# Kernel tuning notes

Measured on AMD Instinct MI355X. Metric: run time of the kernel, lower is better.

Reference implementation:

```python
import jax, jax.numpy as jnp
import numpy as np

N, K = 16384, 32          # num bboxes, context size
IN_F, HID = 608, 384      # in_features, hidden_dim
ALPHA = 0.2               # LeakyReLU slope
NEG_INF = -9e15


def setup_inputs() -> dict:
    key = jax.random.key(0)
    k1, k2, k3, k4, k5, k6, k7, k8 = jax.random.split(key, 8)
    h_i = jax.random.normal(k1, (N, IN_F), dtype=jnp.float32)
    idx = jax.random.randint(k2, (N, K), 0, N)
    pad = jax.random.uniform(k3, (N, K)) < 0.2
    context_indices = jnp.where(pad, -1, idx).astype(jnp.int64)
    s_in = 1.0 / np.sqrt(IN_F)
    s_a = 1.0 / np.sqrt(2 * HID)
    W_i = jax.random.uniform(k4, (IN_F, HID), minval=-s_in, maxval=s_in, dtype=jnp.float32)
    W_j = jax.random.uniform(k5, (IN_F, HID), minval=-s_in, maxval=s_in, dtype=jnp.float32)
    a_i = jax.random.uniform(k6, (HID,), minval=-s_a, maxval=s_a, dtype=jnp.float32)
    a_j = jax.random.uniform(k7, (HID,), minval=-s_a, maxval=s_a, dtype=jnp.float32)
    a_b = jax.random.uniform(k8, (1,), minval=-s_a, maxval=s_a, dtype=jnp.float32)
    return {"h_i": h_i, "context_indices": context_indices,
            "W_i": W_i, "W_j": W_j, "a_i": a_i, "a_j": a_j, "a_b": a_b}


def reference(h_i, context_indices, W_i, W_j, a_i, a_j, a_b):
    n = h_i.shape[0]
    Wh_i = h_i @ W_i                          # [N, H]
    # W_j has no bias, so projecting then gathering (zero pad row) equals
    # gathering zero-padded features then projecting.
    Wh_all = h_i @ W_j                        # [N, H]
    Wh_pad = jnp.concatenate([Wh_all, jnp.zeros((1, HID), Wh_all.dtype)], axis=0)
    idx = jnp.where(context_indices >= 0, context_indices, n)   # -1 -> zero row
    Wh_j = Wh_pad[idx]                        # [N, K, H] gather
    # attention_layer(concat(Wh_i, Wh_j)) == Wh_i@a_i + Wh_j@a_j + b
    scores = (Wh_i @ a_i)[:, None] + Wh_j @ a_j + a_b[0]        # [N, K]
    scores = jnp.where(scores > 0, scores, ALPHA * scores)      # LeakyReLU
    scores = jnp.where(context_indices >= 0, scores, NEG_INF)   # mask padding
    att = jax.nn.softmax(scores, axis=1)                        # [N, K]
    h_prime = jnp.einsum('nk,nkh->nh', att, Wh_j)               # [N, H]
    return h_prime
```

## Files before the change

kernel.cpp:

```cpp
#include <hip/hip_runtime.h>
#include <hip/hip_bf16.h>

typedef unsigned short u16;
typedef unsigned int u32;
typedef __attribute__((ext_vector_type(8))) __bf16 bf16x8;
typedef __attribute__((ext_vector_type(4))) __bf16 bf16x4;
typedef __attribute__((ext_vector_type(4))) float f32x4;

#define KCTX 32
#define INF_ 608
#define HID_ 384

#define WH_OFF  19922944
#define BT_OFF  32505856
#define V_OFF   32972800
#define SI_OFF  32975232
#define SJ_OFF  33040768
#define AJF_OFF 33106304
#define ABF_OFF 33107840

__device__ __forceinline__ float bfu(u16 u)  { return __uint_as_float(((u32)u) << 16); }
__device__ __forceinline__ float bflo(u32 u) { return __uint_as_float(u << 16); }
__device__ __forceinline__ float bfhi(u32 u) { return __uint_as_float(u & 0xffff0000u); }
__device__ __forceinline__ u16 f2bf(float x) {
  u32 u = __float_as_uint(x);
  return (u16)((u + 0x7fffu + ((u >> 16) & 1u)) >> 16);
}
__device__ __forceinline__ void async_ld16(const void* g, void* l) {
  __builtin_amdgcn_global_load_lds(
      (const __attribute__((address_space(1))) u32*)g,
      (__attribute__((address_space(3))) u32*)l, 16, 0, 0);
}

__device__ __forceinline__ int detect_f32(const u32* hw) {
  const u32 w = hw[threadIdx.x & 63];
  const int e = (int)((w >> 7) & 0xffu);
  const unsigned long long mb = __ballot(e > 134 || e < 100);
  return __popcll(mb) >= 16;
}
__device__ __forceinline__ int detect_i64(const int* ci) {
  const int hi = ci[2 * (threadIdx.x & 63) + 1];
  const unsigned long long mz = __ballot(hi == 0 || hi == -1);
  return __popcll(mz) >= 48;
}

__global__ __launch_bounds__(256) void prep_kernel(
    const void* __restrict__ h, const void* __restrict__ Wi,
    const void* __restrict__ Wj, const void* __restrict__ ai,
    const void* __restrict__ aj, const void* __restrict__ ab,
    u16* __restrict__ Bt, float* __restrict__ v, float* __restrict__ sj,
    float* __restrict__ ajf, float* __restrict__ abf) {
  __shared__ u16 tile[64][65];
  const int f32m = detect_f32((const u32*)h);
  const int bid = blockIdx.x, tid = threadIdx.x;
  if (bid < 60) {
    const int ft = bid / 6, ht = bid - ft * 6;
    const int f0 = ft * 64, h0 = ht * 64;
    const int ln = tid & 63, fg = tid >> 6;
#pragma unroll
    for (int rr = 0; rr < 16; ++rr) {
      const int fl = fg * 16 + rr;
      const int f = f0 + fl;
      if (f < INF_)
        tile[fl][ln] = f32m ? f2bf(((const float*)Wj)[(size_t)f * HID_ + h0 + ln])
                            : ((const u16*)Wj)[(size_t)f * HID_ + h0 + ln];
    }
    __syncthreads();
#pragma unroll
    for (int rr = 0; rr < 16; ++rr) {
      const int hl = fg * 16 + rr;
      const int f = f0 + ln;
      if (f < INF_) Bt[(size_t)(h0 + hl) * INF_ + f] = tile[ln][hl];
    }
  } else if (bid < 98) {
    const int t = (bid - 60) * 16 + (tid >> 4);
    const int sl = tid & 15;
    if (t < INF_) {
      float s = 0.f;
      if (f32m) {
        const float4* wi = (const float4*)((const float*)Wi + (size_t)t * HID_);
        const float4* a4 = (const float4*)ai;
        for (int c = sl; c < 96; c += 16) {
          float4 x = wi[c], y = a4[c];
          s += x.x * y.x + x.y * y.y + x.z * y.z + x.w * y.w;
        }
      } else {
        const uint4* wi = (const uint4*)((const u16*)Wi + (size_t)t * HID_);
        const uint4* a4 = (const uint4*)ai;
        for (int c = sl; c < 48; c += 16) {
          uint4 x = wi[c], y = a4[c];
          s += bflo(x.x) * bflo(y.x) + bfhi(x.x) * bfhi(y.x)
             + bflo(x.y) * bflo(y.y) + bfhi(x.y) * bfhi(y.y)
             + bflo(x.z) * bflo(y.z) + bfhi(x.z) * bfhi(y.z)
             + bflo(x.w) * bflo(y.w) + bfhi(x.w) * bfhi(y.w);
        }
      }
      s += __shfl_xor(s, 1); s += __shfl_xor(s, 2);
      s += __shfl_xor(s, 4); s += __shfl_xor(s, 8);
      if (sl == 0) v[t] = s;
    }
  } else {
#pragma unroll 8
    for (int j = 0; j < 64; ++j) sj[j * 256 + tid] = 0.f;
    for (int j = tid; j < HID_; j += 256)
      ajf[j] = f32m ? ((const float*)aj)[j] : bfu(((const u16*)aj)[j]);
    if (tid == 0)
      abf[0] = f32m ? ((const float*)ab)[0] : bfu(((const u16*)ab)[0]);
  }
}

__global__ __launch_bounds__(256) void gemm_fused(
    const void* __restrict__ A,
    const u16* __restrict__ Bt,
    const float* __restrict__ v,
    u16* __restrict__ C,
    float* __restrict__ si, const float* __restrict__ ajf,
    float* __restrict__ sj) {
  __shared__ __align__(16) u16 As[32][612];
  __shared__ __align__(16) u16 Bs[12288];
  const int f32m = detect_f32((const u32*)A);
  const int tid  = threadIdx.x;
  const int lane = tid & 63;
  const int wv   = tid >> 6;
  const int row0 = blockIdx.x * 32;
  const char* Btb = (const char*)Bt;

#pragma unroll
  for (int i = 0; i < 6; ++i) {
    const int c = tid + i * 256;
    async_ld16(Btb + (size_t)(c >> 2) * 1216 + (c & 3) * 16, (char*)Bs + c * 16);
  }

  {
    const int g = tid >> 3, sub = tid & 7;
    float s = 0.f;
    const float4* v4 = (const float4*)v;
    if (f32m) {
      const float4* hr = (const float4*)((const float*)A + (size_t)(row0 + g) * INF_);
#pragma unroll
      for (int k = 0; k < 19; ++k) {
        const int c4 = sub + 8 * k;
        float4 x = hr[c4];
        ushort4 sv;
        sv.x = f2bf(x.x); sv.y = f2bf(x.y); sv.z = f2bf(x.z); sv.w = f2bf(x.w);
        *(ushort4*)&As[g][c4 * 4] = sv;
        float4 w = v4[c4];
        s += x.x * w.x + x.y * w.y + x.z * w.z + x.w * w.w;
      }
    } else {
      const uint4* hr = (const uint4*)((const u16*)A + (size_t)(row0 + g) * INF_);
      for (int k = 0; k < 10; ++k) {
        const int c8 = sub + 8 * k;
        if (c8 < 76) {
          uint4 x = hr[c8];
          *(ushort4*)&As[g][c8 * 8]     = *(ushort4*)&x.x;
          *(ushort4*)&As[g][c8 * 8 + 4] = *(ushort4*)&x.z;
          float4 w0 = v4[2 * c8], w1 = v4[2 * c8 + 1];
          s += bflo(x.x) * w0.x + bfhi(x.x) * w0.y + bflo(x.y) * w0.z + bfhi(x.y) * w0.w
             + bflo(x.z) * w1.x + bfhi(x.z) * w1.y + bflo(x.w) * w1.z + bfhi(x.w) * w1.w;
        }
      }
    }
    s += __shfl_xor(s, 1); s += __shfl_xor(s, 2); s += __shfl_xor(s, 4);
    if (sub == 0) si[row0 + g] = s;
  }

  f32x4 acc[2][6];
#pragma unroll
  for (int i = 0; i < 2; ++i)
#pragma unroll
    for (int j = 0; j < 6; ++j) acc[i][j] = (f32x4){0.f, 0.f, 0.f, 0.f};

  const int lm = lane & 15, q = lane >> 4;
  const int n0 = wv * 96;

  for (int kt = 0; kt < 19; ++kt) {
    __syncthreads();
    bf16x8 af[2], bfr[6];
#pragma unroll
    for (int im = 0; im < 2; ++im) {
      const int r = im * 16 + lm;
      bf16x4 lo = *(const bf16x4*)&As[r][kt * 32 + q * 8];
      bf16x4 hi = *(const bf16x4*)&As[r][kt * 32 + q * 8 + 4];
      af[im] = __builtin_shufflevector(lo, hi, 0, 1, 2, 3, 4, 5, 6, 7);
    }
#pragma unroll
    for (int in = 0; in < 6; ++in)
      bfr[in] = *(const bf16x8*)&Bs[(n0 + in * 16 + lm) * 32 + q * 8];
#pragma unroll
    for (int im = 0; im < 2; ++im)
#pragma unroll
      for (int in = 0; in < 6; ++in)
        acc[im][in] = __builtin_amdgcn_mfma_f32_16x16x32_bf16(
            af[im], bfr[in], acc[im][in], 0, 0, 0);
    __syncthreads();
    if (kt < 18) {
      const size_t kb = (size_t)(kt + 1) * 64;
#pragma unroll
      for (int i = 0; i < 6; ++i) {
        const int c = tid + i * 256;
        async_ld16(Btb + (size_t)(c >> 2) * 1216 + kb + (c & 3) * 16, (char*)Bs + c * 16);
      }
    }
  }

#pragma unroll
  for (int im = 0; im < 2; ++im)
#pragma unroll
    for (int in = 0; in < 6; ++in) {
      const int colg = n0 + in * 16 + lm;
#pragma unroll
      for (int r = 0; r < 4; ++r) {
        const int rowg = row0 + im * 16 + q * 4 + r;
        C[(size_t)rowg * HID_ + colg] = f2bf(acc[im][in][r]);
      }
    }
  float ajv[6];
#pragma unroll
  for (int in = 0; in < 6; ++in) ajv[in] = ajf[n0 + in * 16 + lm];
#pragma unroll
  for (int im = 0; im < 2; ++im)
#pragma unroll
    for (int r = 0; r < 4; ++r) {
      float p = acc[im][0][r] * ajv[0] + acc[im][1][r] * ajv[1]
              + acc[im][2][r] * ajv[2] + acc[im][3][r] * ajv[3]
              + acc[im][4][r] * ajv[4] + acc[im][5][r] * ajv[5];
      p += __shfl_xor(p, 1); p += __shfl_xor(p, 2);
      p += __shfl_xor(p, 4); p += __shfl_xor(p, 8);
      if (lm == 0) atomicAdd(&sj[row0 + im * 16 + q * 4 + r], p);
    }
}

__global__ __launch_bounds__(256) void attn_kernel(
    const void* __restrict__ h, const int* __restrict__ ci,
    const float* __restrict__ si, const float* __restrict__ sj,
    const float* __restrict__ abf, const u16* __restrict__ Wh,
    void* __restrict__ out) {
  const int f32m = detect_f32((const u32*)h);
  const int i64  = detect_i64(ci);
  const int wv = threadIdx.x >> 6, lane = threadIdx.x & 63;
  const int n = blockIdx.x * 4 + wv;

  float att = 0.f; int idxv = 0;
  if (lane < 32) {
    const size_t t = (size_t)n * KCTX + lane;
    int idx;
    if (i64) { int lo = ci[2 * t], hi = ci[2 * t + 1]; idx = (hi < 0) ? -1 : lo; }
    else     { idx = ci[t]; }
    const bool valid = idx >= 0;
    const float sjv = valid ? sj[idx] : 0.f;
    float raw = si[n] + sjv + abf[0];
    float lr = raw > 0.f ? raw : 0.2f * raw;
    float s = valid ? lr : -9e15f;
    float m = s;
#pragma unroll
    for (int o = 16; o; o >>= 1) m = fmaxf(m, __shfl_xor(m, o, 32));
    float p = __expf(s - m);
    float d = p;
#pragma unroll
    for (int o = 16; o; o >>= 1) d += __shfl_xor(d, o, 32);
    att = valid ? p / d : 0.f;
    idxv = valid ? idx : 0;
  }

  if (lane < 48) {
    float a0 = 0, a1 = 0, a2 = 0, a3 = 0, a4 = 0, a5 = 0, a6 = 0, a7 = 0;
#pragma unroll
    for (int kb = 0; kb < KCTX; kb += 8) {
      uint4 q[8]; float ww[8];
#pragma unroll
      for (int u = 0; u < 8; ++u) {
        ww[u] = __shfl(att, kb + u);
        const int j = __shfl(idxv, kb + u);
        q[u] = ((const uint4*)(Wh + (u32)j * HID_))[lane];
      }
#pragma unroll
      for (int u = 0; u < 8; ++u) {
        const float w = ww[u];
        a0 += w * bflo(q[u].x); a1 += w * bfhi(q[u].x);
        a2 += w * bflo(q[u].y); a3 += w * bfhi(q[u].y);
        a4 += w * bflo(q[u].z); a5 += w * bfhi(q[u].z);
        a6 += w * bflo(q[u].w); a7 += w * bfhi(q[u].w);
      }
    }
    if (f32m) {
      float4* o4 = (float4*)out + (size_t)n * 96 + lane * 2;
      o4[0] = (float4){a0, a1, a2, a3};
      o4[1] = (float4){a4, a5, a6, a7};
    } else {
      uint4 o;
      o.x = (u32)f2bf(a0) | ((u32)f2bf(a1) << 16);
      o.y = (u32)f2bf(a2) | ((u32)f2bf(a3) << 16);
      o.z = (u32)f2bf(a4) | ((u32)f2bf(a5) << 16);
      o.w = (u32)f2bf(a6) | ((u32)f2bf(a7) << 16);
      ((uint4*)out)[(size_t)n * 48 + lane] = o;
    }
  }
}

extern "C" void kernel_launch(void* const* d_in, const int* in_sizes, int n_in,
                              void* d_out, int out_size, void* d_ws, size_t ws_size,
                              hipStream_t stream) {
  const void* h  = d_in[0];
  const int*  ci = (const int*)d_in[1];
  const void* Wi = d_in[2];
  const void* Wj = d_in[3];
  const void* ai = d_in[4];
  const void* aj = d_in[5];
  const void* ab = d_in[6];

  char* ws = (char*)d_ws;
  u16*   Wh  = (u16*)(ws + WH_OFF);
  u16*   Bt  = (u16*)(ws + BT_OFF);
  float* v   = (float*)(ws + V_OFF);
  float* si  = (float*)(ws + SI_OFF);
  float* sj  = (float*)(ws + SJ_OFF);
  float* ajf = (float*)(ws + AJF_OFF);
  float* abf = (float*)(ws + ABF_OFF);

  prep_kernel<<<99, 256, 0, stream>>>(h, Wi, Wj, ai, aj, ab, Bt, v, sj, ajf, abf);
  gemm_fused<<<512, 256, 0, stream>>>(h, Bt, v, Wh, si, ajf, sj);
  attn_kernel<<<4096, 256, 0, stream>>>(h, ci, si, sj, abf, Wh, d_out);
}
```

Measured before the change: 156.7 us.

## Compact valid context entries and pack five rows per attention block

```diff
diff --git a/kernel.cpp b/kernel.cpp
--- a/kernel.cpp
+++ b/kernel.cpp
@@ -10,6 +10,7 @@
 #define KCTX 32
 #define INF_ 608
 #define HID_ 384
+#define NBOX 16384
 
 #define WH_OFF  19922944
 #define BT_OFF  32505856
@@ -110,10 +111,8 @@
 }
 
 __global__ __launch_bounds__(256) void gemm_fused(
-    const void* __restrict__ A,
-    const u16* __restrict__ Bt,
-    const float* __restrict__ v,
-    u16* __restrict__ C,
+    const void* __restrict__ A, const u16* __restrict__ Bt,
+    const float* __restrict__ v, u16* __restrict__ C,
     float* __restrict__ si, const float* __restrict__ ajf,
     float* __restrict__ sj) {
   __shared__ __align__(16) u16 As[32][612];
@@ -236,64 +235,85 @@
     const float* __restrict__ si, const float* __restrict__ sj,
     const float* __restrict__ abf, const u16* __restrict__ Wh,
     void* __restrict__ out) {
+  __shared__ float2 ai_c[5][32];
+  __shared__ int cnt_s[5];
   const int f32m = detect_f32((const u32*)h);
   const int i64  = detect_i64(ci);
-  const int wv = threadIdx.x >> 6, lane = threadIdx.x & 63;
-  const int n = blockIdx.x * 4 + wv;
-
-  float att = 0.f; int idxv = 0;
-  if (lane < 32) {
-    const size_t t = (size_t)n * KCTX + lane;
-    int idx;
-    if (i64) { int lo = ci[2 * t], hi = ci[2 * t + 1]; idx = (hi < 0) ? -1 : lo; }
-    else     { idx = ci[t]; }
-    const bool valid = idx >= 0;
-    const float sjv = valid ? sj[idx] : 0.f;
-    float raw = si[n] + sjv + abf[0];
-    float lr = raw > 0.f ? raw : 0.2f * raw;
-    float s = valid ? lr : -9e15f;
-    float m = s;
-#pragma unroll
-    for (int o = 16; o; o >>= 1) m = fmaxf(m, __shfl_xor(m, o, 32));
-    float p = __expf(s - m);
-    float d = p;
-#pragma unroll
-    for (int o = 16; o; o >>= 1) d += __shfl_xor(d, o, 32);
-    att = valid ? p / d : 0.f;
-    idxv = valid ? idx : 0;
-  }
-
-  if (lane < 48) {
-    float a0 = 0, a1 = 0, a2 = 0, a3 = 0, a4 = 0, a5 = 0, a6 = 0, a7 = 0;
-#pragma unroll
-    for (int kb = 0; kb < KCTX; kb += 8) {
-      uint4 q[8]; float ww[8];
-#pragma unroll
-      for (int u = 0; u < 8; ++u) {
-        ww[u] = __shfl(att, kb + u);
-        const int j = __shfl(idxv, kb + u);
-        q[u] = ((const uint4*)(Wh + (u32)j * HID_))[lane];
-      }
-#pragma unroll
-      for (int u = 0; u < 8; ++u) {
-        const float w = ww[u];
-        a0 += w * bflo(q[u].x); a1 += w * bfhi(q[u].x);
-        a2 += w * bflo(q[u].y); a3 += w * bfhi(q[u].y);
-        a4 += w * bflo(q[u].z); a5 += w * bfhi(q[u].z);
-        a6 += w * bflo(q[u].w); a7 += w * bfhi(q[u].w);
-      }
-    }
-    if (f32m) {
-      float4* o4 = (float4*)out + (size_t)n * 96 + lane * 2;
-      o4[0] = (float4){a0, a1, a2, a3};
-      o4[1] = (float4){a4, a5, a6, a7};
-    } else {
-      uint4 o;
-      o.x = (u32)f2bf(a0) | ((u32)f2bf(a1) << 16);
-      o.y = (u32)f2bf(a2) | ((u32)f2bf(a3) << 16);
-      o.z = (u32)f2bf(a4) | ((u32)f2bf(a5) << 16);
-      o.w = (u32)f2bf(a6) | ((u32)f2bf(a7) << 16);
-      ((uint4*)out)[(size_t)n * 48 + lane] = o;
+  const int tid = threadIdx.x;
+  const int n0 = blockIdx.x * 5;
+
+  if (tid < 160) {
+    const int r = tid >> 5, k = tid & 31;
+    const int n = n0 + r;
+    if (n < NBOX) {
+      const size_t t = (size_t)n * KCTX + k;
+      int idx;
+      if (i64) { int lo = ci[2 * t], hi2 = ci[2 * t + 1]; idx = (hi2 < 0) ? -1 : lo; }
+      else     { idx = ci[t]; }
+      const bool valid = idx >= 0;
+      const float sjv = valid ? sj[idx] : 0.f;
+      float raw = si[n] + sjv + abf[0];
+      float lr = raw > 0.f ? raw : 0.2f * raw;
+      float s = valid ? lr : -9e15f;
+      float m = s;
+#pragma unroll
+      for (int o = 16; o; o >>= 1) m = fmaxf(m, __shfl_xor(m, o, 32));
+      float p = __expf(s - m);
+      float d = p;
+#pragma unroll
+      for (int o = 16; o; o >>= 1) d += __shfl_xor(d, o, 32);
+      const unsigned long long bm = __ballot(valid);
+      const u32 m32 = (u32)(bm >> (tid & 32));
+      const int cnt = __popc(m32);
+      const int r8 = (cnt + 7) & ~7;
+      if (valid) {
+        const int pf = __popc(m32 & ((1u << k) - 1u));
+        ai_c[r][pf] = (float2){p / d, __int_as_float(idx)};
+      }
+      if (k >= cnt && k < r8) ai_c[r][k] = (float2){0.f, 0.f};
+      if (k == 0) cnt_s[r] = r8;
+    } else if ((tid & 31) == 0) {
+      cnt_s[r] = 0;
+    }
+  }
+  __syncthreads();
+
+  if (tid < 240) {
+    const int r = tid / 48, c = tid - r * 48;
+    const int n = n0 + r;
+    if (n < NBOX) {
+      const int K8 = cnt_s[r];
+      float a0 = 0, a1 = 0, a2 = 0, a3 = 0, a4 = 0, a5 = 0, a6 = 0, a7 = 0;
+      for (int kb = 0; kb < K8; kb += 8) {
+        uint4 q[8]; float ww[8];
+#pragma unroll
+        for (int u = 0; u < 8; ++u) {
+          const float2 e = ai_c[r][kb + u];
+          ww[u] = e.x;
+          const int j = __float_as_int(e.y);
+          q[u] = ((const uint4*)(Wh + (u32)j * HID_))[c];
+        }
+#pragma unroll
+        for (int u = 0; u < 8; ++u) {
+          const float w = ww[u];
+          a0 += w * bflo(q[u].x); a1 += w * bfhi(q[u].x);
+          a2 += w * bflo(q[u].y); a3 += w * bfhi(q[u].y);
+          a4 += w * bflo(q[u].z); a5 += w * bfhi(q[u].z);
+          a6 += w * bflo(q[u].w); a7 += w * bfhi(q[u].w);
+        }
+      }
+      if (f32m) {
+        float4* o4 = (float4*)out + (size_t)n * 96 + c * 2;
+        o4[0] = (float4){a0, a1, a2, a3};
+        o4[1] = (float4){a4, a5, a6, a7};
+      } else {
+        uint4 o;
+        o.x = (u32)f2bf(a0) | ((u32)f2bf(a1) << 16);
+        o.y = (u32)f2bf(a2) | ((u32)f2bf(a3) << 16);
+        o.z = (u32)f2bf(a4) | ((u32)f2bf(a5) << 16);
+        o.w = (u32)f2bf(a6) | ((u32)f2bf(a7) << 16);
+        ((uint4*)out)[(size_t)n * 48 + c] = o;
+      }
     }
   }
 }
@@ -320,5 +340,5 @@
 
   prep_kernel<<<99, 256, 0, stream>>>(h, Wi, Wj, ai, aj, ab, Bt, v, sj, ajf, abf);
   gemm_fused<<<512, 256, 0, stream>>>(h, Bt, v, Wh, si, ajf, sj);
-  attn_kernel<<<4096, 256, 0, stream>>>(h, ci, si, sj, abf, Wh, d_out);
-}
+  attn_kernel<<<3277, 256, 0, stream>>>(h, ci, si, sj, abf, Wh, d_out);
+}
```

After: 156.8 us (median of 2 runs). No clear change (+0.1%).

## Split score softmax into own kernel and slice Wh gather by column chunks

Applied to the files above, without the earlier changes.

```diff
diff --git a/kernel.cpp b/kernel.cpp
--- a/kernel.cpp
+++ b/kernel.cpp
@@ -6,18 +6,23 @@
 typedef __attribute__((ext_vector_type(8))) __bf16 bf16x8;
 typedef __attribute__((ext_vector_type(4))) __bf16 bf16x4;
 typedef __attribute__((ext_vector_type(4))) float f32x4;
+typedef __attribute__((ext_vector_type(2))) float f32x2;
+typedef __attribute__((ext_vector_type(4))) u32 u32x4;
 
 #define KCTX 32
 #define INF_ 608
 #define HID_ 384
-
-#define WH_OFF  19922944
-#define BT_OFF  32505856
-#define V_OFF   32972800
-#define SI_OFF  32975232
-#define SJ_OFF  33040768
-#define AJF_OFF 33106304
-#define ABF_OFF 33107840
+#define NBOX 16384
+#define WSTR 512
+
+#define WHP_OFF  0
+#define BT_OFF   16777216
+#define V_OFF    17244160
+#define SI_OFF   17246592
+#define SJ_OFF   17312128
+#define AJF_OFF  17377664
+#define ABF_OFF  17379200
+#define ATTP_OFF 17379264
 
 __device__ __forceinline__ float bfu(u16 u)  { return __uint_as_float(((u32)u) << 16); }
 __device__ __forceinline__ float bflo(u32 u) { return __uint_as_float(u << 16); }
@@ -110,10 +115,8 @@
 }
 
 __global__ __launch_bounds__(256) void gemm_fused(
-    const void* __restrict__ A,
-    const u16* __restrict__ Bt,
-    const float* __restrict__ v,
-    u16* __restrict__ C,
+    const void* __restrict__ A, const u16* __restrict__ Bt,
+    const float* __restrict__ v, u16* __restrict__ C,
     float* __restrict__ si, const float* __restrict__ ajf,
     float* __restrict__ sj) {
   __shared__ __align__(16) u16 As[32][612];
@@ -208,11 +211,13 @@
   for (int im = 0; im < 2; ++im)
 #pragma unroll
     for (int in = 0; in < 6; ++in) {
-      const int colg = n0 + in * 16 + lm;
+      const int cb = in * 16 + lm;
+      const int slc = wv * 2 + (in >= 3 ? 1 : 0);
+      const int cc  = cb - (in >= 3 ? 48 : 0);
 #pragma unroll
       for (int r = 0; r < 4; ++r) {
         const int rowg = row0 + im * 16 + q * 4 + r;
-        C[(size_t)rowg * HID_ + colg] = f2bf(acc[im][in][r]);
+        C[(size_t)rowg * WSTR + slc * 64 + cc] = f2bf(acc[im][in][r]);
       }
     }
   float ajv[6];
@@ -231,48 +236,71 @@
     }
 }
 
+__global__ __launch_bounds__(256) void score_kernel(
+    const int* __restrict__ ci, const float* __restrict__ si,
+    const float* __restrict__ sj, const float* __restrict__ abf,
+    f32x2* __restrict__ attp) {
+  const int i64 = detect_i64(ci);
+  const int r = threadIdx.x >> 5, k = threadIdx.x & 31;
+  const int n = blockIdx.x * 8 + r;
+  const size_t t = (size_t)n * KCTX + k;
+  int idx;
+  if (i64) { int lo = ci[2 * t], hi = ci[2 * t + 1]; idx = (hi < 0) ? -1 : lo; }
+  else     { idx = ci[t]; }
+  const bool valid = idx >= 0;
+  const float sjv = valid ? sj[idx] : 0.f;
+  float raw = si[n] + sjv + abf[0];
+  float lr = raw > 0.f ? raw : 0.2f * raw;
+  float s = valid ? lr : -9e15f;
+  float m = s;
+#pragma unroll
+  for (int o = 16; o; o >>= 1) m = fmaxf(m, __shfl_xor(m, o, 32));
+  float p = __expf(s - m);
+  float d = p;
+#pragma unroll
+  for (int o = 16; o; o >>= 1) d += __shfl_xor(d, o, 32);
+  f32x2 e;
+  e.x = valid ? p / d : 0.f;
+  e.y = __int_as_float(valid ? idx : 0);
+  __builtin_nontemporal_store(e, &attp[t]);
+}
+
 __global__ __launch_bounds__(256) void attn_kernel(
-    const void* __restrict__ h, const int* __restrict__ ci,
-    const float* __restrict__ si, const float* __restrict__ sj,
-    const float* __restrict__ abf, const u16* __restrict__ Wh,
-    void* __restrict__ out) {
+    const void* __restrict__ h, const f32x2* __restrict__ attp,
+    const u16* __restrict__ Whp, void* __restrict__ out) {
+  __shared__ f32x2 att_s[40][33];
   const int f32m = detect_f32((const u32*)h);
-  const int i64  = detect_i64(ci);
-  const int wv = threadIdx.x >> 6, lane = threadIdx.x & 63;
-  const int n = blockIdx.x * 4 + wv;
-
-  float att = 0.f; int idxv = 0;
-  if (lane < 32) {
-    const size_t t = (size_t)n * KCTX + lane;
-    int idx;
-    if (i64) { int lo = ci[2 * t], hi = ci[2 * t + 1]; idx = (hi < 0) ? -1 : lo; }
-    else     { idx = ci[t]; }
-    const bool valid = idx >= 0;
-    const float sjv = valid ? sj[idx] : 0.f;
-    float raw = si[n] + sjv + abf[0];
-    float lr = raw > 0.f ? raw : 0.2f * raw;
-    float s = valid ? lr : -9e15f;
-    float m = s;
-#pragma unroll
-    for (int o = 16; o; o >>= 1) m = fmaxf(m, __shfl_xor(m, o, 32));
-    float p = __expf(s - m);
-    float d = p;
-#pragma unroll
-    for (int o = 16; o; o >>= 1) d += __shfl_xor(d, o, 32);
-    att = valid ? p / d : 0.f;
-    idxv = valid ? idx : 0;
-  }
-
-  if (lane < 48) {
+  const int tid = threadIdx.x;
+  const int slc = blockIdx.x & 7;
+  const int n0 = (blockIdx.x >> 3) * 40;
+
+#pragma unroll
+  for (int i = 0; i < 5; ++i) {
+    const int e = tid + i * 256;
+    const int rr = e >> 5, kk = e & 31;
+    f32x2 val = (f32x2){0.f, 0.f};
+    if (n0 + rr < NBOX)
+      val = __builtin_nontemporal_load(&attp[(size_t)n0 * KCTX + e]);
+    att_s[rr][kk] = val;
+  }
+  __syncthreads();
+
+  const int wv = tid >> 6, lane = tid & 63;
+  if (lane < 60) {
+    const int rr = lane / 6, cc = lane - rr * 6;
+    const int lr = wv * 10 + rr;
+    const int n = n0 + lr;
+    const u16* base = Whp + slc * 64 + cc * 8;
     float a0 = 0, a1 = 0, a2 = 0, a3 = 0, a4 = 0, a5 = 0, a6 = 0, a7 = 0;
 #pragma unroll
     for (int kb = 0; kb < KCTX; kb += 8) {
       uint4 q[8]; float ww[8];
 #pragma unroll
       for (int u = 0; u < 8; ++u) {
-        ww[u] = __shfl(att, kb + u);
-        const int j = __shfl(idxv, kb + u);
-        q[u] = ((const uint4*)(Wh + (u32)j * HID_))[lane];
+        const f32x2 e = att_s[lr][kb + u];
+        ww[u] = e.x;
+        const u32 j = (u32)__float_as_int(e.y);
+        q[u] = *(const uint4*)(base + (size_t)j * WSTR);
       }
 #pragma unroll
       for (int u = 0; u < 8; ++u) {
@@ -283,17 +311,20 @@
         a6 += w * bflo(q[u].w); a7 += w * bfhi(q[u].w);
       }
     }
-    if (f32m) {
-      float4* o4 = (float4*)out + (size_t)n * 96 + lane * 2;
-      o4[0] = (float4){a0, a1, a2, a3};
-      o4[1] = (float4){a4, a5, a6, a7};
-    } else {
-      uint4 o;
-      o.x = (u32)f2bf(a0) | ((u32)f2bf(a1) << 16);
-      o.y = (u32)f2bf(a2) | ((u32)f2bf(a3) << 16);
-      o.z = (u32)f2bf(a4) | ((u32)f2bf(a5) << 16);
-      o.w = (u32)f2bf(a6) | ((u32)f2bf(a7) << 16);
-      ((uint4*)out)[(size_t)n * 48 + lane] = o;
+    if (n < NBOX) {
+      const int c0 = slc * 48 + cc * 8;
+      if (f32m) {
+        float* op = (float*)out + (size_t)n * HID_ + c0;
+        __builtin_nontemporal_store((f32x4){a0, a1, a2, a3}, (f32x4*)op);
+        __builtin_nontemporal_store((f32x4){a4, a5, a6, a7}, (f32x4*)(op + 4));
+      } else {
+        u32x4 o;
+        o.x = (u32)f2bf(a0) | ((u32)f2bf(a1) << 16);
+        o.y = (u32)f2bf(a2) | ((u32)f2bf(a3) << 16);
+        o.z = (u32)f2bf(a4) | ((u32)f2bf(a5) << 16);
+        o.w = (u32)f2bf(a6) | ((u32)f2bf(a7) << 16);
+        __builtin_nontemporal_store(o, (u32x4*)((u16*)out + (size_t)n * HID_ + c0));
+      }
     }
   }
 }
@@ -310,15 +341,17 @@
   const void* ab = d_in[6];
 
   char* ws = (char*)d_ws;
-  u16*   Wh  = (u16*)(ws + WH_OFF);
-  u16*   Bt  = (u16*)(ws + BT_OFF);
-  float* v   = (float*)(ws + V_OFF);
-  float* si  = (float*)(ws + SI_OFF);
-  float* sj  = (float*)(ws + SJ_OFF);
-  float* ajf = (float*)(ws + AJF_OFF);
-  float* abf = (float*)(ws + ABF_OFF);
+  u16*   Whp  = (u16*)(ws + WHP_OFF);
+  u16*   Bt   = (u16*)(ws + BT_OFF);
+  float* v    = (float*)(ws + V_OFF);
+  float* si   = (float*)(ws + SI_OFF);
+  float* sj   = (float*)(ws + SJ_OFF);
+  float* ajf  = (float*)(ws + AJF_OFF);
+  float* abf  = (float*)(ws + ABF_OFF);
+  f32x2* attp = (f32x2*)(ws + ATTP_OFF);
 
   prep_kernel<<<99, 256, 0, stream>>>(h, Wi, Wj, ai, aj, ab, Bt, v, sj, ajf, abf);
-  gemm_fused<<<512, 256, 0, stream>>>(h, Bt, v, Wh, si, ajf, sj);
-  attn_kernel<<<4096, 256, 0, stream>>>(h, ci, si, sj, abf, Wh, d_out);
-}
+  gemm_fused<<<512, 256, 0, stream>>>(h, Bt, v, Whp, si, ajf, sj);
+  score_kernel<<<2048, 256, 0, stream>>>(ci, si, sj, abf, attp);
+  attn_kernel<<<3280, 256, 0, stream>>>(h, attp, Whp, d_out);
+}
```

After: 164.9 us. +5.2%, slower.
